# Optimization experiments

Hardware: AMD Instinct MI355X
Metric: run time of the kernel (lower is better)

The kernel has to match this reference:

```python
import jax, jax.numpy as jnp
import numpy as np

NEG_SLOPE = 0.2


def gat_layer(x, src, dst, W, a_src, a_dst, b, concat):
    # x: [N, F_in], W: [F_in, H*C], a_src/a_dst: [H, C], b: [H*C] or [C]
    N = x.shape[0]
    H, C = a_src.shape
    h = (x @ W).reshape(N, H, C)                       # per-head projections
    al_s = jnp.einsum('nhc,hc->nh', h, a_src)          # [N, H]
    al_d = jnp.einsum('nhc,hc->nh', h, a_dst)          # [N, H]
    e = jax.nn.leaky_relu(al_s[src] + al_d[dst], NEG_SLOPE)  # [E, H]
    # softmax over incoming edges of each destination node
    m = jax.ops.segment_max(e, dst, num_segments=N)    # [N, H]
    ex = jnp.exp(e - m[dst])
    s = jax.ops.segment_sum(ex, dst, num_segments=N)   # [N, H]
    alpha = ex / (s[dst] + 1e-16)                      # [E, H]
    msg = h[src] * alpha[:, :, None]                   # [E, H, C]
    out = jax.ops.segment_sum(msg, dst, num_segments=N)  # [N, H, C]
    out = out.reshape(N, H * C) if concat else out.mean(axis=1)
    return out + b


def setup_inputs() -> dict:
    key = jax.random.key(0)
    ks = jax.random.split(key, 12)
    N, E, F_in, HID, H, NCLS = 100000, 1600000, 128, 32, 4, 40
    x = jax.random.normal(ks[0], (N, F_in), dtype=jnp.float32)
    edge_index = jax.random.randint(ks[1], (2, E), 0, N, dtype=jnp.int32)
    W1 = jax.random.normal(ks[2], (F_in, H * HID), dtype=jnp.float32) * 0.1
    as1 = jax.random.normal(ks[3], (H, HID), dtype=jnp.float32) * 0.1
    ad1 = jax.random.normal(ks[4], (H, HID), dtype=jnp.float32) * 0.1
    b1 = jnp.zeros((H * HID,), dtype=jnp.float32)
    W2 = jax.random.normal(ks[5], (H * HID, H * NCLS), dtype=jnp.float32) * 0.1
    as2 = jax.random.normal(ks[6], (H, NCLS), dtype=jnp.float32) * 0.1
    ad2 = jax.random.normal(ks[7], (H, NCLS), dtype=jnp.float32) * 0.1
    b2 = jnp.zeros((NCLS,), dtype=jnp.float32)
    return {"x": x, "edge_index": edge_index, "W1": W1, "as1": as1,
            "ad1": ad1, "b1": b1, "W2": W2, "as2": as2, "ad2": ad2, "b2": b2}


def reference(x, edge_index, W1, as1, ad1, b1, W2, as2, ad2, b2):
    src, dst = edge_index[0], edge_index[1]
    h = gat_layer(x, src, dst, W1, as1, ad1, b1, concat=True)
    h = jax.nn.relu(h)  # dropout=0.0 -> identity
    out = gat_layer(h, src, dst, W2, as2, ad2, b2, concat=False)
    return jax.nn.log_softmax(out, axis=-1)
```

## Files before the change

kernel.cpp:

```cpp
#include <hip/hip_runtime.h>

typedef short short8 __attribute__((ext_vector_type(8)));
typedef float f32x4 __attribute__((ext_vector_type(4)));
typedef int   i32x4 __attribute__((ext_vector_type(4)));
typedef unsigned short u16;
typedef unsigned int u32;

__device__ __forceinline__ float b2f(u16 u){ union{u32 i; float f;} v; v.i=((u32)u)<<16; return v.f; }
__device__ __forceinline__ u16 f2b(float f){ union{float f; u32 i;} v; v.f=f; return (u16)((v.i + 0x7fffu + ((v.i>>16)&1u))>>16); }
__device__ __forceinline__ float loadv(const void* p, long i, bool isbf){
  return isbf ? b2f(((const u16*)p)[i]) : ((const float*)p)[i];
}
__device__ __forceinline__ float wred(float v){
  v += __shfl_xor(v, 1); v += __shfl_xor(v, 2); v += __shfl_xor(v, 4);
  v += __shfl_xor(v, 8); v += __shfl_xor(v, 16); v += __shfl_xor(v, 32);
  return v;
}

__global__ void detect_bf16(const void* x, int n, int* flag){
  __shared__ int cnt;
  if (threadIdx.x==0) cnt = 0;
  __syncthreads();
  int m = n < 4096 ? n : 4096;
  int good = 0;
  for (int i = threadIdx.x; i < m; i += 256){
    u16 u = ((const u16*)x)[i];
    int e = (u >> 7) & 0xff;
    if (u == 0 || (e >= 100 && e <= 140)) good++;
  }
  atomicAdd(&cnt, good);
  __syncthreads();
  if (threadIdx.x==0){
    flag[0] = (cnt >= (m*3)/4) ? 1 : 0;
    flag[1] = 1;
  }
}

__global__ __launch_bounds__(256) void count_x(const int* __restrict__ dst,
    int* __restrict__ counts, int E, int N, int nchunk){
  int r = blockIdx.x & 7;
  int chunk = blockIdx.x >> 3;
  int lo = (int)(((long)N * r) >> 3);
  int hi = (int)(((long)N * (r+1)) >> 3);
  int per = (E + nchunk - 1) / nchunk;
  int s = chunk * per, t = min(E, s + per);
  for (int e = s + threadIdx.x; e < t; e += 256){
    int d = dst[e];
    if (d >= lo && d < hi) atomicAdd(&counts[d], 1);
  }
}

__global__ __launch_bounds__(256) void scatter_x(const int* __restrict__ src, const int* __restrict__ dst,
    const int* __restrict__ rp, int* __restrict__ cur,
    int* __restrict__ psrc, int E, int N, int nchunk){
  int r = blockIdx.x & 7;
  int chunk = blockIdx.x >> 3;
  int lo = (int)(((long)N * r) >> 3);
  int hi = (int)(((long)N * (r+1)) >> 3);
  int per = (E + nchunk - 1) / nchunk;
  int s = chunk * per, t = min(E, s + per);
  for (int e = s + threadIdx.x; e < t; e += 256){
    int d = dst[e];
    if (d >= lo && d < hi){
      int pos = rp[d] + atomicAdd(&cur[d], 1);
      psrc[pos] = src[e];
    }
  }
}

__global__ __launch_bounds__(256) void scan_bsum(const int* __restrict__ counts, int* __restrict__ bsum, int N){
  __shared__ int sm[256];
  int t = threadIdx.x, i = blockIdx.x*256 + t;
  sm[t] = (i < N) ? counts[i] : 0;
  __syncthreads();
  for (int off = 128; off; off >>= 1){
    if (t < off) sm[t] += sm[t+off];
    __syncthreads();
  }
  if (t == 0) bsum[blockIdx.x] = sm[0];
}

__global__ __launch_bounds__(1024) void scan_top(const int* __restrict__ bsum, int* __restrict__ bscan, int B){
  __shared__ int sm[1024];
  int t = threadIdx.x;
  int v = (t < B) ? bsum[t] : 0;
  sm[t] = v;
  __syncthreads();
  for (int off = 1; off < 1024; off <<= 1){
    int x = (t >= off) ? sm[t-off] : 0;
    __syncthreads();
    sm[t] += x;
    __syncthreads();
  }
  if (t < B) bscan[t] = sm[t] - v;
}

__global__ __launch_bounds__(256) void scan_final(const int* __restrict__ counts, const int* __restrict__ bscan,
                                                  int* __restrict__ rp, int N, int E){
  __shared__ int sm[256];
  int t = threadIdx.x, i = blockIdx.x*256 + t;
  int v = (i < N) ? counts[i] : 0;
  sm[t] = v;
  __syncthreads();
  for (int off = 1; off < 256; off <<= 1){
    int x = (t >= off) ? sm[t-off] : 0;
    __syncthreads();
    sm[t] += x;
    __syncthreads();
  }
  if (i < N) rp[i] = bscan[blockIdx.x] + sm[t] - v;
  if (i == 0) rp[N] = E;
}

template<int M>
__global__ __launch_bounds__(256) void gemm_k(const void* __restrict__ X, const void* __restrict__ W,
                                              u16* __restrict__ OUT, int N,
                                              const int* __restrict__ flagX, const int* __restrict__ flagW){
  __shared__ u16 wt[M][136];
  const bool xbf = *flagX != 0;
  const bool wbf = *flagW != 0;
  int tid = threadIdx.x;
  for (int i = tid; i < 128*M; i += 256){
    int k = i / M, c = i % M;
    wt[c][k] = wbf ? ((const u16*)W)[i] : f2b(((const float*)W)[i]);
  }
  __syncthreads();
  int wave = tid >> 6, lane = tid & 63;
  int quad = lane >> 4, l16 = lane & 15;
  int rowbase = blockIdx.x*64 + wave*16;
  int rr = rowbase + l16; if (rr >= N) rr = N-1;
  const int NT = M/16;
  f32x4 acc[NT];
  #pragma unroll
  for (int t=0;t<NT;t++) acc[t] = (f32x4){0.f,0.f,0.f,0.f};
  #pragma unroll
  for (int kt = 0; kt < 4; kt++){
    int kb = kt*32 + quad*8;
    short8 a;
    if (xbf){
      a = *(const short8*)((const u16*)X + (size_t)rr*128 + kb);
    } else {
      const float* xf = (const float*)X + (size_t)rr*128 + kb;
      #pragma unroll
      for (int j=0;j<8;j++) a[j] = (short)f2b(xf[j]);
    }
    #pragma unroll
    for (int t=0;t<NT;t++){
      short8 b = *(const short8*)&wt[t*16 + l16][kb];
      acc[t] = __builtin_amdgcn_mfma_f32_16x16x32_bf16(a, b, acc[t], 0, 0, 0);
    }
  }
  #pragma unroll
  for (int t=0;t<NT;t++){
    #pragma unroll
    for (int r=0;r<4;r++){
      int row = rowbase + quad*4 + r;
      if (row < N) OUT[(size_t)row*M + t*16 + l16] = f2b(acc[t][r]);
    }
  }
}

template<int C>
__global__ __launch_bounds__(256) void al_k(const u16* __restrict__ Hm, const void* __restrict__ as_,
                     const void* __restrict__ ad_,
                     float* __restrict__ als, float* __restrict__ ald, int N, const int* __restrict__ flag){
  __shared__ float s_as[4*C], s_ad[4*C];
  const bool isbf = *flag != 0;
  for (int i = threadIdx.x; i < 4*C; i += 256){
    s_as[i] = loadv(as_, i, isbf);
    s_ad[i] = loadv(ad_, i, isbf);
  }
  __syncthreads();
  int idx = blockIdx.x*256 + threadIdx.x;
  if (idx >= N*4) return;
  int n = idx >> 2, h = idx & 3;
  const short8* row = (const short8*)(Hm + (size_t)n*(4*C) + h*C);
  float ss = 0.f, sd = 0.f;
  #pragma unroll
  for (int v = 0; v < C/8; v++){
    short8 pk = row[v];
    #pragma unroll
    for (int j = 0; j < 8; j++){
      union{u32 i; float f;} u; u.i = ((u32)(u16)pk[j]) << 16;
      ss += u.f * s_as[h*C + v*8 + j];
      sd += u.f * s_ad[h*C + v*8 + j];
    }
  }
  als[idx] = ss;
  ald[idx] = sd;
}

__global__ __launch_bounds__(256) void agg1(const u16* __restrict__ h1,
    const float* __restrict__ als, const float* __restrict__ ald, const void* __restrict__ b1,
    const int* __restrict__ rp, const int* __restrict__ psrc,
    u16* __restrict__ hrelu, int N, const int* __restrict__ flag){
  __shared__ int   sbuf[4][64];
  __shared__ float ebT[4][4*68];
  const bool isbf = *flag != 0;
  int wave = threadIdx.x >> 6, lane = threadIdx.x & 63;
  int node = blockIdx.x*4 + wave;
  bool live = node < N;
  int nd = live ? node : 0;
  int hd = lane >> 4;
  int beg = __builtin_amdgcn_readfirstlane(rp[nd]);
  int end = __builtin_amdgcn_readfirstlane(rp[nd+1]);
  if (!live){ beg = 0; end = 0; }
  f32x4 adv = *(const f32x4*)(ald + nd*4);
  const char* hb = (const char*)h1;
  int lane4 = lane << 2;
  int* sb = sbuf[wave];
  float* eb = ebT[wave];
  float a0 = 0.f, a1 = 0.f;
  float sp0 = 0.f, sp1 = 0.f, sp2 = 0.f, sp3 = 0.f;
  for (int cbeg = beg; cbeg < end; cbeg += 64){
    int cnt = min(64, end - cbeg);
    int cnt4 = (cnt + 3) & ~3;
    int e = cbeg + lane;
    if (e < end){
      int s = psrc[e];
      f32x4 av = *(const f32x4*)(als + s*4);
      float l0 = av[0]+adv[0], l1 = av[1]+adv[1], l2 = av[2]+adv[2], l3 = av[3]+adv[3];
      l0 = fmaxf(l0, 0.2f*l0); l1 = fmaxf(l1, 0.2f*l1);
      l2 = fmaxf(l2, 0.2f*l2); l3 = fmaxf(l3, 0.2f*l3);
      float e0 = __expf(l0), e1 = __expf(l1), e2 = __expf(l2), e3 = __expf(l3);
      sp0 += e0; sp1 += e1; sp2 += e2; sp3 += e3;
      sb[lane] = s << 8;
      eb[0*68 + lane] = e0; eb[1*68 + lane] = e1;
      eb[2*68 + lane] = e2; eb[3*68 + lane] = e3;
    } else if (lane < cnt4){
      sb[lane] = 0;
      eb[0*68 + lane] = 0.f; eb[1*68 + lane] = 0.f;
      eb[2*68 + lane] = 0.f; eb[3*68 + lane] = 0.f;
    }
    for (int j0 = 0; j0 < cnt; j0 += 4){
      i32x4 off4 = *(const i32x4*)&sb[j0];
      f32x4 ex4  = *(const f32x4*)&eb[hd*68 + j0];
      u32 p[4];
      #pragma unroll
      for (int i=0;i<4;i++) p[i] = *(const u32*)(hb + (u32)(off4[i] + lane4));
      #pragma unroll
      for (int i=0;i<4;i++){
        union{u32 u; float f;} w;
        w.u = p[i] << 16;         a0 += ex4[i]*w.f;
        w.u = p[i] & 0xffff0000u; a1 += ex4[i]*w.f;
      }
    }
  }
  float s0 = wred(sp0), s1 = wred(sp1), s2 = wred(sp2), s3 = wred(sp3);
  float sum = hd == 0 ? s0 : hd == 1 ? s1 : hd == 2 ? s2 : s3;
  if (live){
    float inv = 1.f/(sum + 1e-16f);
    float v0 = a0*inv + loadv(b1, 2*lane,     isbf);
    float v1 = a1*inv + loadv(b1, 2*lane + 1, isbf);
    v0 = v0 > 0.f ? v0 : 0.f;
    v1 = v1 > 0.f ? v1 : 0.f;
    u32 packed = (u32)f2b(v0) | ((u32)f2b(v1) << 16);
    *(u32*)(hrelu + (size_t)node*128 + 2*lane) = packed;
  }
}

__global__ __launch_bounds__(256) void agg2(const u16* __restrict__ h2,
    const float* __restrict__ als, const float* __restrict__ ald, const void* __restrict__ b2,
    const int* __restrict__ rp, const int* __restrict__ psrc,
    void* __restrict__ out, int N, const int* __restrict__ flag){
  __shared__ int   sbuf[4][64];
  __shared__ float ebT[4][4*68];
  __shared__ float sm[4][160];
  const bool isbf = *flag != 0;
  int wave = threadIdx.x >> 6, lane = threadIdx.x & 63;
  int node = blockIdx.x*4 + wave;
  bool live = node < N;
  int nd = live ? node : 0;
  int hA = lane / 20;
  bool hasB = lane < 16;
  int beg = __builtin_amdgcn_readfirstlane(rp[nd]);
  int end = __builtin_amdgcn_readfirstlane(rp[nd+1]);
  if (!live){ beg = 0; end = 0; }
  f32x4 adv = *(const f32x4*)(ald + nd*4);
  const char* hb = (const char*)h2;
  int lane4 = lane << 2;
  int* sb = sbuf[wave];
  float* eb = ebT[wave];
  float aA0 = 0.f, aA1 = 0.f, aB0 = 0.f, aB1 = 0.f;
  float sp0 = 0.f, sp1 = 0.f, sp2 = 0.f, sp3 = 0.f;
  for (int cbeg = beg; cbeg < end; cbeg += 64){
    int cnt = min(64, end - cbeg);
    int cnt4 = (cnt + 3) & ~3;
    int e = cbeg + lane;
    if (e < end){
      int s = psrc[e];
      f32x4 av = *(const f32x4*)(als + s*4);
      float l0 = av[0]+adv[0], l1 = av[1]+adv[1], l2 = av[2]+adv[2], l3 = av[3]+adv[3];
      l0 = fmaxf(l0, 0.2f*l0); l1 = fmaxf(l1, 0.2f*l1);
      l2 = fmaxf(l2, 0.2f*l2); l3 = fmaxf(l3, 0.2f*l3);
      float e0 = __expf(l0), e1 = __expf(l1), e2 = __expf(l2), e3 = __expf(l3);
      sp0 += e0; sp1 += e1; sp2 += e2; sp3 += e3;
      sb[lane] = s * 320;
      eb[0*68 + lane] = e0; eb[1*68 + lane] = e1;
      eb[2*68 + lane] = e2; eb[3*68 + lane] = e3;
    } else if (lane < cnt4){
      sb[lane] = 0;
      eb[0*68 + lane] = 0.f; eb[1*68 + lane] = 0.f;
      eb[2*68 + lane] = 0.f; eb[3*68 + lane] = 0.f;
    }
    for (int j0 = 0; j0 < cnt; j0 += 4){
      i32x4 off4 = *(const i32x4*)&sb[j0];
      f32x4 exA4 = *(const f32x4*)&eb[hA*68 + j0];
      f32x4 exB4 = *(const f32x4*)&eb[3*68 + j0];
      u32 p[4], q[4];
      #pragma unroll
      for (int i=0;i<4;i++){
        u32 vo = (u32)(off4[i] + lane4);
        p[i] = *(const u32*)(hb + vo);
        if (hasB) q[i] = *(const u32*)(hb + vo + 256);
      }
      #pragma unroll
      for (int i=0;i<4;i++){
        union{u32 u; float f;} w;
        w.u = p[i] << 16;         aA0 += exA4[i]*w.f;
        w.u = p[i] & 0xffff0000u; aA1 += exA4[i]*w.f;
        if (hasB){
          w.u = q[i] << 16;         aB0 += exB4[i]*w.f;
          w.u = q[i] & 0xffff0000u; aB1 += exB4[i]*w.f;
        }
      }
    }
  }
  float s0 = wred(sp0), s1 = wred(sp1), s2 = wred(sp2), s3 = wred(sp3);
  float sumA = hA == 0 ? s0 : hA == 1 ? s1 : hA == 2 ? s2 : s3;
  float invA = 1.f/(sumA + 1e-16f);
  sm[wave][2*lane]     = aA0*invA;
  sm[wave][2*lane + 1] = aA1*invA;
  if (hasB){
    float invB = 1.f/(s3 + 1e-16f);
    sm[wave][128 + 2*lane] = aB0*invB;
    sm[wave][129 + 2*lane] = aB1*invB;
  }
  __syncthreads();
  float v = -__builtin_inff();
  if (lane < 40)
    v = (sm[wave][lane] + sm[wave][40+lane] + sm[wave][80+lane] + sm[wave][120+lane]) * 0.25f
        + loadv(b2, lane, isbf);
  float mxo = v;
  for (int o = 32; o; o >>= 1) mxo = fmaxf(mxo, __shfl_xor(mxo, o));
  float ex = (lane < 40) ? __expf(v - mxo) : 0.f;
  float S = ex;
  for (int o = 32; o; o >>= 1) S += __shfl_xor(S, o);
  if (live && lane < 40){
    float r = v - mxo - __logf(S);
    if (isbf) ((u16*)out)[(size_t)node*40 + lane] = f2b(r);
    else      ((float*)out)[(size_t)node*40 + lane] = r;
  }
}

extern "C" void kernel_launch(void* const* d_in, const int* in_sizes, int n_in,
                              void* d_out, int out_size, void* d_ws, size_t ws_size,
                              hipStream_t stream){
  const void* x   = d_in[0];
  const int*  ei  = (const int*)d_in[1];
  const void* W1  = d_in[2];
  const void* as1 = d_in[3];
  const void* ad1 = d_in[4];
  const void* b1  = d_in[5];
  const void* W2  = d_in[6];
  const void* as2 = d_in[7];
  const void* ad2 = d_in[8];
  const void* b2  = d_in[9];

  const int N = in_sizes[0] / 128;
  const int E = in_sizes[1] / 2;
  const int* esrc = ei;
  const int* edst = ei + E;

  char* w = (char*)d_ws;
  size_t off = 0;
  auto take = [&](size_t bytes)->void*{
    void* p = w + off;
    off = (off + bytes + 255) & ~(size_t)255;
    return p;
  };
  u16*   h12    = (u16*)take((size_t)N*160*2);
  u16*   hrelu  = (u16*)take((size_t)N*128*2);
  float* als1   = (float*)take((size_t)N*4*4);
  float* ald1   = (float*)take((size_t)N*4*4);
  float* als2   = (float*)take((size_t)N*4*4);
  float* ald2   = (float*)take((size_t)N*4*4);
  int*   rowptr = (int*)take((size_t)(N+1)*4);
  int*   counts = (int*)take((size_t)N*4);
  int*   bsum   = (int*)take(1024*4);
  int*   bscan  = (int*)take(1024*4);
  int*   psrc   = (int*)take((size_t)E*4);
  int*   flag   = (int*)take(64);

  const int B = (N + 255) / 256;
  const int NCHUNK = 128;

  detect_bf16<<<1, 256, 0, stream>>>(x, N*128, flag);

  hipMemsetAsync(counts, 0, (size_t)N*4, stream);
  count_x<<<8*NCHUNK, 256, 0, stream>>>(edst, counts, E, N, NCHUNK);
  scan_bsum<<<B, 256, 0, stream>>>(counts, bsum, N);
  scan_top<<<1, 1024, 0, stream>>>(bsum, bscan, B);
  scan_final<<<B, 256, 0, stream>>>(counts, bscan, rowptr, N, E);
  hipMemsetAsync(counts, 0, (size_t)N*4, stream);
  scatter_x<<<8*NCHUNK, 256, 0, stream>>>(esrc, edst, rowptr, counts, psrc, E, N, NCHUNK);

  gemm_k<128><<<(N+63)/64, 256, 0, stream>>>(x, W1, h12, N, flag, flag);
  al_k<32><<<(4*N+255)/256, 256, 0, stream>>>(h12, as1, ad1, als1, ald1, N, flag);
  agg1<<<(N+3)/4, 256, 0, stream>>>(h12, als1, ald1, b1, rowptr, psrc, hrelu, N, flag);

  gemm_k<160><<<(N+63)/64, 256, 0, stream>>>(hrelu, W2, h12, N, flag+1, flag);
  al_k<40><<<(4*N+255)/256, 256, 0, stream>>>(h12, as2, ad2, als2, ald2, N, flag);
  agg2<<<(N+3)/4, 256, 0, stream>>>(h12, als2, ald2, b2, rowptr, psrc, d_out, N, flag);
}
```

Before: 561.7 us.

## Pretranspose weights once and restructure edge aggregation to 16-edge chunks

Adds a convw kernel that converts and transposes W1/W2 to bf16 once, so each GEMM block copies weights into LDS with vectorized loads instead of strided scalar conversion. agg1 and agg2 now process edges in 16-edge chunks, with each lane computing one (edge, head) attention logit, which replaces four exps per lane and removes the padding logic. agg2 remaps lanes so four groups of 16 lanes each handle a different edge using 16-byte loads, then combine partial sums with cross-lane shuffles. This aims to cut idle lanes on low-degree nodes and reduce gather instructions, at the cost of extra shuffle reductions and more chunk iterations for high-degree nodes.

After: 486.8 us. 1.15x faster.

```diff
diff --git a/kernel.cpp b/kernel.cpp
--- a/kernel.cpp
+++ b/kernel.cpp
@@ -10,11 +10,6 @@
 __device__ __forceinline__ u16 f2b(float f){ union{float f; u32 i;} v; v.f=f; return (u16)((v.i + 0x7fffu + ((v.i>>16)&1u))>>16); }
 __device__ __forceinline__ float loadv(const void* p, long i, bool isbf){
   return isbf ? b2f(((const u16*)p)[i]) : ((const float*)p)[i];
-}
-__device__ __forceinline__ float wred(float v){
-  v += __shfl_xor(v, 1); v += __shfl_xor(v, 2); v += __shfl_xor(v, 4);
-  v += __shfl_xor(v, 8); v += __shfl_xor(v, 16); v += __shfl_xor(v, 32);
-  return v;
 }
 
 __global__ void detect_bf16(const void* x, int n, int* flag){
@@ -34,6 +29,15 @@
     flag[0] = (cnt >= (m*3)/4) ? 1 : 0;
     flag[1] = 1;
   }
+}
+
+__global__ __launch_bounds__(256) void convw(const void* __restrict__ W, u16* __restrict__ WT,
+                                             int M, const int* __restrict__ flag){
+  const bool wbf = *flag != 0;
+  int i = blockIdx.x*256 + threadIdx.x;
+  if (i >= 128*M) return;
+  int k = i / M, c = i - k*M;
+  WT[c*128 + k] = wbf ? ((const u16*)W)[i] : f2b(((const float*)W)[i]);
 }
 
 __global__ __launch_bounds__(256) void count_x(const int* __restrict__ dst,
@@ -113,16 +117,15 @@
 }
 
 template<int M>
-__global__ __launch_bounds__(256) void gemm_k(const void* __restrict__ X, const void* __restrict__ W,
+__global__ __launch_bounds__(256) void gemm_k(const void* __restrict__ X, const u16* __restrict__ WT,
                                               u16* __restrict__ OUT, int N,
-                                              const int* __restrict__ flagX, const int* __restrict__ flagW){
+                                              const int* __restrict__ flagX){
   __shared__ u16 wt[M][136];
   const bool xbf = *flagX != 0;
-  const bool wbf = *flagW != 0;
   int tid = threadIdx.x;
-  for (int i = tid; i < 128*M; i += 256){
-    int k = i / M, c = i % M;
-    wt[c][k] = wbf ? ((const u16*)W)[i] : f2b(((const float*)W)[i]);
+  for (int i = tid; i < M*16; i += 256){
+    int c = i >> 4, k8 = (i & 15) << 3;
+    *(short8*)&wt[c][k8] = *(const short8*)&WT[c*128 + k8];
   }
   __syncthreads();
   int wave = tid >> 6, lane = tid & 63;
@@ -194,47 +197,40 @@
     const float* __restrict__ als, const float* __restrict__ ald, const void* __restrict__ b1,
     const int* __restrict__ rp, const int* __restrict__ psrc,
     u16* __restrict__ hrelu, int N, const int* __restrict__ flag){
-  __shared__ int   sbuf[4][64];
-  __shared__ float ebT[4][4*68];
+  __shared__ __align__(16) int   sbuf[4][16];
+  __shared__ __align__(16) float ebT[4][4*20];
   const bool isbf = *flag != 0;
   int wave = threadIdx.x >> 6, lane = threadIdx.x & 63;
   int node = blockIdx.x*4 + wave;
   bool live = node < N;
   int nd = live ? node : 0;
   int hd = lane >> 4;
+  int eidx = lane >> 2, hA = lane & 3;
   int beg = __builtin_amdgcn_readfirstlane(rp[nd]);
   int end = __builtin_amdgcn_readfirstlane(rp[nd+1]);
   if (!live){ beg = 0; end = 0; }
-  f32x4 adv = *(const f32x4*)(ald + nd*4);
+  float advA = ald[nd*4 + hA];
   const char* hb = (const char*)h1;
   int lane4 = lane << 2;
   int* sb = sbuf[wave];
   float* eb = ebT[wave];
   float a0 = 0.f, a1 = 0.f;
-  float sp0 = 0.f, sp1 = 0.f, sp2 = 0.f, sp3 = 0.f;
-  for (int cbeg = beg; cbeg < end; cbeg += 64){
-    int cnt = min(64, end - cbeg);
-    int cnt4 = (cnt + 3) & ~3;
-    int e = cbeg + lane;
-    if (e < end){
-      int s = psrc[e];
-      f32x4 av = *(const f32x4*)(als + s*4);
-      float l0 = av[0]+adv[0], l1 = av[1]+adv[1], l2 = av[2]+adv[2], l3 = av[3]+adv[3];
-      l0 = fmaxf(l0, 0.2f*l0); l1 = fmaxf(l1, 0.2f*l1);
-      l2 = fmaxf(l2, 0.2f*l2); l3 = fmaxf(l3, 0.2f*l3);
-      float e0 = __expf(l0), e1 = __expf(l1), e2 = __expf(l2), e3 = __expf(l3);
-      sp0 += e0; sp1 += e1; sp2 += e2; sp3 += e3;
-      sb[lane] = s << 8;
-      eb[0*68 + lane] = e0; eb[1*68 + lane] = e1;
-      eb[2*68 + lane] = e2; eb[3*68 + lane] = e3;
-    } else if (lane < cnt4){
-      sb[lane] = 0;
-      eb[0*68 + lane] = 0.f; eb[1*68 + lane] = 0.f;
-      eb[2*68 + lane] = 0.f; eb[3*68 + lane] = 0.f;
-    }
+  float sp = 0.f;
+  for (int cbeg = beg; cbeg < end; cbeg += 16){
+    int cnt = min(16, end - cbeg);
+    int e = cbeg + eidx;
+    bool vv = e < end;
+    int ec = vv ? e : beg;
+    int s = psrc[ec];
+    float lv = als[s*4 + hA] + advA;
+    lv = fmaxf(lv, 0.2f*lv);
+    float ex = vv ? __expf(lv) : 0.f;
+    sp += ex;
+    eb[hA*20 + eidx] = ex;
+    if (hA == 0) sb[eidx] = vv ? (s << 8) : 0;
     for (int j0 = 0; j0 < cnt; j0 += 4){
       i32x4 off4 = *(const i32x4*)&sb[j0];
-      f32x4 ex4  = *(const f32x4*)&eb[hd*68 + j0];
+      f32x4 ex4  = *(const f32x4*)&eb[hd*20 + j0];
       u32 p[4];
       #pragma unroll
       for (int i=0;i<4;i++) p[i] = *(const u32*)(hb + (u32)(off4[i] + lane4));
@@ -246,8 +242,9 @@
       }
     }
   }
-  float s0 = wred(sp0), s1 = wred(sp1), s2 = wred(sp2), s3 = wred(sp3);
-  float sum = hd == 0 ? s0 : hd == 1 ? s1 : hd == 2 ? s2 : s3;
+  sp += __shfl_xor(sp, 4);  sp += __shfl_xor(sp, 8);
+  sp += __shfl_xor(sp, 16); sp += __shfl_xor(sp, 32);
+  float sum = __shfl(sp, hd);
   if (live){
     float inv = 1.f/(sum + 1e-16f);
     float v0 = a0*inv + loadv(b1, 2*lane,     isbf);
@@ -263,78 +260,75 @@
     const float* __restrict__ als, const float* __restrict__ ald, const void* __restrict__ b2,
     const int* __restrict__ rp, const int* __restrict__ psrc,
     void* __restrict__ out, int N, const int* __restrict__ flag){
-  __shared__ int   sbuf[4][64];
-  __shared__ float ebT[4][4*68];
-  __shared__ float sm[4][160];
+  __shared__ __align__(16) int   sbuf[4][16];
+  __shared__ __align__(16) float ebT[4][4*20];
+  __shared__ __align__(16) float sm[4][160];
   const bool isbf = *flag != 0;
   int wave = threadIdx.x >> 6, lane = threadIdx.x & 63;
   int node = blockIdx.x*4 + wave;
   bool live = node < N;
   int nd = live ? node : 0;
-  int hA = lane / 20;
-  bool hasB = lane < 16;
+  int g = lane >> 4, s = lane & 15;
+  int hm = s / 5;
+  int moff = s << 4;
+  int toff = 256 + (s << 2);
+  int eidx = lane >> 2, hA = lane & 3;
   int beg = __builtin_amdgcn_readfirstlane(rp[nd]);
   int end = __builtin_amdgcn_readfirstlane(rp[nd+1]);
   if (!live){ beg = 0; end = 0; }
-  f32x4 adv = *(const f32x4*)(ald + nd*4);
+  float advA = ald[nd*4 + hA];
   const char* hb = (const char*)h2;
-  int lane4 = lane << 2;
   int* sb = sbuf[wave];
   float* eb = ebT[wave];
-  float aA0 = 0.f, aA1 = 0.f, aB0 = 0.f, aB1 = 0.f;
-  float sp0 = 0.f, sp1 = 0.f, sp2 = 0.f, sp3 = 0.f;
-  for (int cbeg = beg; cbeg < end; cbeg += 64){
-    int cnt = min(64, end - cbeg);
-    int cnt4 = (cnt + 3) & ~3;
-    int e = cbeg + lane;
-    if (e < end){
-      int s = psrc[e];
-      f32x4 av = *(const f32x4*)(als + s*4);
-      float l0 = av[0]+adv[0], l1 = av[1]+adv[1], l2 = av[2]+adv[2], l3 = av[3]+adv[3];
-      l0 = fmaxf(l0, 0.2f*l0); l1 = fmaxf(l1, 0.2f*l1);
-      l2 = fmaxf(l2, 0.2f*l2); l3 = fmaxf(l3, 0.2f*l3);
-      float e0 = __expf(l0), e1 = __expf(l1), e2 = __expf(l2), e3 = __expf(l3);
-      sp0 += e0; sp1 += e1; sp2 += e2; sp3 += e3;
-      sb[lane] = s * 320;
-      eb[0*68 + lane] = e0; eb[1*68 + lane] = e1;
-      eb[2*68 + lane] = e2; eb[3*68 + lane] = e3;
-    } else if (lane < cnt4){
-      sb[lane] = 0;
-      eb[0*68 + lane] = 0.f; eb[1*68 + lane] = 0.f;
-      eb[2*68 + lane] = 0.f; eb[3*68 + lane] = 0.f;
-    }
+  float am[8] = {0.f,0.f,0.f,0.f,0.f,0.f,0.f,0.f};
+  float at0 = 0.f, at1 = 0.f;
+  float sp = 0.f;
+  for (int cbeg = beg; cbeg < end; cbeg += 16){
+    int cnt = min(16, end - cbeg);
+    int e = cbeg + eidx;
+    bool vv = e < end;
+    int ec = vv ? e : beg;
+    int src = psrc[ec];
+    float lv = als[src*4 + hA] + advA;
+    lv = fmaxf(lv, 0.2f*lv);
+    float ex = vv ? __expf(lv) : 0.f;
+    sp += ex;
+    eb[hA*20 + eidx] = ex;
+    if (hA == 0) sb[eidx] = vv ? src*320 : 0;
     for (int j0 = 0; j0 < cnt; j0 += 4){
-      i32x4 off4 = *(const i32x4*)&sb[j0];
-      f32x4 exA4 = *(const f32x4*)&eb[hA*68 + j0];
-      f32x4 exB4 = *(const f32x4*)&eb[3*68 + j0];
-      u32 p[4], q[4];
+      int off   = sb[j0 + g];
+      float exm = eb[hm*20 + j0 + g];
+      float ext = eb[3*20  + j0 + g];
+      i32x4 P = *(const i32x4*)(hb + (u32)(off + moff));
+      u32   q = *(const u32*) (hb + (u32)(off + toff));
+      union{u32 u; float f;} w;
       #pragma unroll
       for (int i=0;i<4;i++){
-        u32 vo = (u32)(off4[i] + lane4);
-        p[i] = *(const u32*)(hb + vo);
-        if (hasB) q[i] = *(const u32*)(hb + vo + 256);
+        u32 pv = (u32)P[i];
+        w.u = pv << 16;         am[2*i]   += exm*w.f;
+        w.u = pv & 0xffff0000u; am[2*i+1] += exm*w.f;
       }
-      #pragma unroll
-      for (int i=0;i<4;i++){
-        union{u32 u; float f;} w;
-        w.u = p[i] << 16;         aA0 += exA4[i]*w.f;
-        w.u = p[i] & 0xffff0000u; aA1 += exA4[i]*w.f;
-        if (hasB){
-          w.u = q[i] << 16;         aB0 += exB4[i]*w.f;
-          w.u = q[i] & 0xffff0000u; aB1 += exB4[i]*w.f;
-        }
-      }
-    }
-  }
-  float s0 = wred(sp0), s1 = wred(sp1), s2 = wred(sp2), s3 = wred(sp3);
-  float sumA = hA == 0 ? s0 : hA == 1 ? s1 : hA == 2 ? s2 : s3;
-  float invA = 1.f/(sumA + 1e-16f);
-  sm[wave][2*lane]     = aA0*invA;
-  sm[wave][2*lane + 1] = aA1*invA;
-  if (hasB){
-    float invB = 1.f/(s3 + 1e-16f);
-    sm[wave][128 + 2*lane] = aB0*invB;
-    sm[wave][129 + 2*lane] = aB1*invB;
+      w.u = q << 16;         at0 += ext*w.f;
+      w.u = q & 0xffff0000u; at1 += ext*w.f;
+    }
+  }
+  sp += __shfl_xor(sp, 4);  sp += __shfl_xor(sp, 8);
+  sp += __shfl_xor(sp, 16); sp += __shfl_xor(sp, 32);
+  float Sm = __shfl(sp, hm);
+  float S3 = __shfl(sp, 3);
+  #pragma unroll
+  for (int k=0;k<8;k++){ am[k] += __shfl_xor(am[k],16); am[k] += __shfl_xor(am[k],32); }
+  at0 += __shfl_xor(at0,16); at0 += __shfl_xor(at0,32);
+  at1 += __shfl_xor(at1,16); at1 += __shfl_xor(at1,32);
+  if (lane < 16){
+    float invm = 1.f/(Sm + 1e-16f);
+    float invt = 1.f/(S3 + 1e-16f);
+    f32x4 v0 = {am[0]*invm, am[1]*invm, am[2]*invm, am[3]*invm};
+    f32x4 v1 = {am[4]*invm, am[5]*invm, am[6]*invm, am[7]*invm};
+    *(f32x4*)&sm[wave][8*s]     = v0;
+    *(f32x4*)&sm[wave][8*s + 4] = v1;
+    sm[wave][128 + 2*s] = at0*invt;
+    sm[wave][129 + 2*s] = at1*invt;
   }
   __syncthreads();
   float v = -__builtin_inff();
@@ -391,11 +385,15 @@
   int*   bscan  = (int*)take(1024*4);
   int*   psrc   = (int*)take((size_t)E*4);
   int*   flag   = (int*)take(64);
+  u16*   wt1    = (u16*)take(128*128*2);
+  u16*   wt2    = (u16*)take(160*128*2);
 
   const int B = (N + 255) / 256;
   const int NCHUNK = 128;
 
   detect_bf16<<<1, 256, 0, stream>>>(x, N*128, flag);
+  convw<<<(128*128+255)/256, 256, 0, stream>>>(W1, wt1, 128, flag);
+  convw<<<(128*160+255)/256, 256, 0, stream>>>(W2, wt2, 160, flag);
 
   hipMemsetAsync(counts, 0, (size_t)N*4, stream);
   count_x<<<8*NCHUNK, 256, 0, stream>>>(edst, counts, E, N, NCHUNK);
@@ -405,11 +403,11 @@
   hipMemsetAsync(counts, 0, (size_t)N*4, stream);
   scatter_x<<<8*NCHUNK, 256, 0, stream>>>(esrc, edst, rowptr, counts, psrc, E, N, NCHUNK);
 
-  gemm_k<128><<<(N+63)/64, 256, 0, stream>>>(x, W1, h12, N, flag, flag);
+  gemm_k<128><<<(N+63)/64, 256, 0, stream>>>(x, wt1, h12, N, flag);
   al_k<32><<<(4*N+255)/256, 256, 0, stream>>>(h12, as1, ad1, als1, ald1, N, flag);
   agg1<<<(N+3)/4, 256, 0, stream>>>(h12, als1, ald1, b1, rowptr, psrc, hrelu, N, flag);
 
-  gemm_k<160><<<(N+63)/64, 256, 0, stream>>>(hrelu, W2, h12, N, flag+1, flag);
+  gemm_k<160><<<(N+63)/64, 256, 0, stream>>>(hrelu, wt2, h12, N, flag+1);
   al_k<40><<<(4*N+255)/256, 256, 0, stream>>>(h12, as2, ad2, als2, ald2, N, flag);
   agg2<<<(N+3)/4, 256, 0, stream>>>(h12, als2, ald2, b2, rowptr, psrc, d_out, N, flag);
 }
```
